# Kernel optimization log

Hardware: AMD Instinct MI355X
Metric: run time of the kernel (lower is better)

Reference implementation:

```python
import jax, jax.numpy as jnp
import numpy as np

NUM_BEAM, NUM_NULL, NUM_BIN, NUM_CH = 8, 4, 257, 8
NUM_BLOCK, NUM_FRAME = 8, 500
ALPHA, LOW_FREQ, HIGH_FREQ = 0.35, 5, 70


def setup_inputs() -> dict:
    key = jax.random.key(0)
    k1, k2, k3, k4 = jax.random.split(key, 4)
    return {
        "input": jax.random.normal(k1, (NUM_BLOCK, NUM_FRAME, 2, NUM_BIN, NUM_CH), jnp.float32),
        "beam_id": jax.random.randint(k2, (NUM_BLOCK,), 0, NUM_BEAM),
        "targ_w": jax.random.normal(k3, (NUM_BEAM, 2, NUM_BIN, NUM_CH), jnp.float32),
        "null_w": jax.random.normal(k4, (NUM_BEAM, NUM_NULL, 2, NUM_BIN, NUM_CH), jnp.float32),
    }


def _forward(input, beam_id, targ_w, null_w):
    a = ALPHA
    xr, xi = input[:, :, 0], input[:, :, 1]            # (B,T,F,C)
    # target beamformer: select per-block complex weights (B,2,F,C)
    tw = targ_w[beam_id]
    twr, twi = tw[:, 0], tw[:, 1]                      # (B,F,C)
    tr = jnp.einsum('btfc,bfc->btf', xr, twr) - jnp.einsum('btfc,bfc->btf', xi, twi)
    ti = jnp.einsum('btfc,bfc->btf', xr, twi) + jnp.einsum('btfc,bfc->btf', xi, twr)
    tr, ti = tr[..., None], ti[..., None]              # (B,T,F,1)
    # null beamformer: (B,N,2,F,C)
    nw = null_w[beam_id]
    nwr, nwi = nw[:, :, 0], nw[:, :, 1]                # (B,N,F,C)
    nr = jnp.einsum('btfc,bnfc->btfn', xr, nwr) - jnp.einsum('btfc,bnfc->btfn', xi, nwi)
    ni = jnp.einsum('btfc,bnfc->btfn', xr, nwi) + jnp.einsum('btfc,bnfc->btfn', xi, nwr)
    # elementwise cross-spectra products (B,T,F,N)
    pr = tr * nr + ti * ni
    pi = ti * nr - tr * ni
    pw = jnp.mean(xr ** 2 + xi ** 2, axis=-1, keepdims=True)  # (B,T,F,1)

    # t = 0 (note: (1-alpha) scales only the FIRST product, as in the source)
    phi_r0 = (1.0 - a) * tr[:, 0] * nr[:, 0] + ti[:, 0] * ni[:, 0]
    phi_i0 = (1.0 - a) * ti[:, 0] * nr[:, 0] - tr[:, 0] * ni[:, 0]
    psd0 = (1.0 - a) * pw[:, 0]
    phi0 = jnp.sqrt(phi_r0 ** 2 + phi_i0 ** 2)
    dcf0 = jnp.clip(phi0 / (psd0 + 1e-13), 0.01, 1.0)

    def step(carry, xs):
        phi_r, phi_i, psd = carry
        pr_t, pi_t, pw_t = xs
        phi_r = a * phi_r + (1.0 - a) * pr_t
        phi_i = a * phi_i + (1.0 - a) * pi_t
        psd = a * psd + (1.0 - a) * pw_t
        phi = jnp.sqrt(phi_r ** 2 + phi_i ** 2)
        dcf_t = jnp.clip(phi / (psd + 1e-13), 0.01, 1.0)
        pre = jnp.sum(psd[:, LOW_FREQ:HIGH_FREQ, :], axis=1, keepdims=True)
        aft = jnp.sum(phi[:, LOW_FREQ:HIGH_FREQ, :], axis=1, keepdims=True)
        ratio = jnp.clip(aft / (pre + 1e-10), 0.01, 1.0)
        dcf_t = jnp.sqrt(dcf_t * ratio)
        return (phi_r, phi_i, psd), dcf_t

    xs = (jnp.moveaxis(pr[:, 1:], 1, 0),
          jnp.moveaxis(pi[:, 1:], 1, 0),
          jnp.moveaxis(pw[:, 1:], 1, 0))
    _, dcf_rest = jax.lax.scan(step, (phi_r0, phi_i0, psd0), xs)  # (T-1,B,F,N)
    dcf = jnp.concatenate([dcf0[None], dcf_rest], axis=0)
    dcf = jnp.moveaxis(dcf, 0, 1)                                 # (B,T,F,N)
    targ_out = jnp.stack([tr[..., 0], ti[..., 0]], axis=2)        # (B,T,2,F)
    return dcf, targ_out


def reference(input, beam_id, targ_w, null_w):
    return _forward(input, beam_id, targ_w, null_w)
```

## Files before the change

kernel.cpp:

```cpp
#include <hip/hip_runtime.h>

#define NB 8
#define NT 500
#define NF 257
#define NC 8
#define NNUL 4
#define LOWF 5
#define HIGHF 70
#define S_CHUNK 8
#define WARM 4
#define N_CHUNK 63
#define AL 0.35f

__device__ __forceinline__ float dot4(const float4& a, const float4& b) {
    return a.x*b.x + a.y*b.y + a.z*b.z + a.w*b.w;
}
__device__ __forceinline__ float dot8(const float4& a0, const float4& a1,
                                      const float4& b0, const float4& b1) {
    return dot4(a0, b0) + dot4(a1, b1);
}
__device__ __forceinline__ float fast_rcp(float v) {
#if __has_builtin(__builtin_amdgcn_rcpf)
    return __builtin_amdgcn_rcpf(v);
#else
    return 1.0f / v;
#endif
}
__device__ __forceinline__ float fast_sqrt(float v) {
#if __has_builtin(__builtin_amdgcn_sqrtf)
    return __builtin_amdgcn_sqrtf(v);
#else
    return sqrtf(v);
#endif
}
__device__ __forceinline__ float clamp01(float v) {
#if __has_builtin(__builtin_amdgcn_fmed3f)
    return __builtin_amdgcn_fmed3f(v, 0.01f, 1.0f);
#else
    return fminf(fmaxf(v, 0.01f), 1.0f);
#endif
}

__global__ __launch_bounds__(1024, 4) void dcf_fused_kernel(
    const float* __restrict__ x,
    const int* __restrict__ beam_id,
    const float* __restrict__ targ_w,
    const float* __restrict__ null_w,
    float* __restrict__ out)
{
    const int tid = threadIdx.x;
    const int bid = blockIdx.x;
    const int b  = bid & 7;
    const int k  = bid >> 3;
    const int t0 = k * S_CHUNK;
    const int te = min(NT, t0 + S_CHUNK);
    int ts = t0 - WARM; if (ts < 0) ts = 0;

    const int f = tid >> 2;
    const int n = tid & 3;
    const int wid = tid >> 6;
    const int lane = tid & 63;
    const bool extra = (tid >= 1020);

    __shared__ float s_w256[16 + 4 * 16];
    __shared__ float s_xe[12 * 16];
    __shared__ float s_part[S_CHUNK][25];
    __shared__ float s_psd[S_CHUNK][260];
    __shared__ float s_dcf[S_CHUNK][1028];

    const int beam = beam_id[b];
    const int pA = n & 1;
    const int offA = pA * (NF * NC);
    const int offB = (1 - pA) * (NF * NC);
    const int psel = (n == 1 || n == 2) ? 1 : 0;
    const float nsign = pA ? -1.f : 1.f;
    const int rl = 2 * NF * NC;

    float4 tw0, tw1, w10, w11, w20, w21, w30, w31, w40, w41;
    {
        const float* tp = targ_w + ((size_t)(beam * 2 + psel) * NF + f) * NC;
        tw0 = *(const float4*)(tp);  tw1 = *(const float4*)(tp + 4);
        const float* qp  = null_w + ((size_t)((beam * NNUL + n) * 2) * NF + f) * NC;
        const float* qpx = null_w + ((size_t)((beam * NNUL + (n ^ 1)) * 2) * NF + f) * NC;
        w10 = *(const float4*)(qp  + offA);  w11 = *(const float4*)(qp  + offA + 4);
        w20 = *(const float4*)(qp  + offB);  w21 = *(const float4*)(qp  + offB + 4);
        w30 = *(const float4*)(qpx + offA);  w31 = *(const float4*)(qpx + offA + 4);
        w40 = *(const float4*)(qpx + offB);  w41 = *(const float4*)(qpx + offB + 4);
    }
    if (tid < 16) {
        int p = tid >> 3, c = tid & 7;
        s_w256[tid] = targ_w[((size_t)(beam * 2 + p) * NF + 256) * NC + c];
    } else if (tid < 80) {
        int i = tid - 16;
        int nn = i >> 4, p = (i >> 3) & 1, c = i & 7;
        s_w256[tid] = null_w[((size_t)((beam * NNUL + nn) * 2 + p) * NF + 256) * NC + c];
    } else if (tid >= 128 && tid < 176) {
        const int i = tid - 128;
        const int c = i >> 1, h = i & 1;
        const int fr = c >> 1, p = c & 1;
        if (fr < te - ts) {
            const float* src = x + (size_t)(b * NT + ts + fr) * rl
                             + p * (NF * NC) + 256 * NC + h * 4;
            *(float4*)&s_xe[fr * 16 + p * 8 + h * 4] = *(const float4*)src;
        }
    }
    __syncthreads();

    float phi_r = 0.f, phi_i = 0.f, psd = 0.f;
    float phi_r2 = 0.f, phi_i2 = 0.f, psd2 = 0.f;
    const float a = AL, oma = 1.0f - AL;

    const float* xpa = x + (size_t)(b * NT + ts) * rl + f * NC + offA;
    float4 pA0 = *(const float4*)(xpa);
    float4 pA1 = *(const float4*)(xpa + 4);

    float* outT = out + (size_t)NB * NT * NF * NNUL;
    float* poT = outT + ((size_t)(b * NT + t0) * 2 + n) * NF + f;
    float* sdp = &s_dcf[0][tid];
    float* spq = &s_psd[0][f];

    for (int t = ts; t < te; ++t) {
        const float4 A0 = pA0, A1 = pA1;
        xpa += rl;
        if (t + 1 < te) {
            pA0 = *(const float4*)(xpa);
            pA1 = *(const float4*)(xpa + 4);
        }

        const float d = dot8(A0, A1, tw0, tw1);
        const float e = __shfl_xor(d, 1);
        const float u = (n < 2) ? ((n == 0) ? (d - e) : (e - d)) : (d + e);
        const float v = __shfl_xor(u, 2);
        const float tr = (n < 2) ? u : v;
        const float ti = (n < 2) ? v : u;

        const float P  = dot8(A0, A1, w10, w11);
        const float X  = dot8(A0, A1, w20, w21);
        const float s3 = dot8(A0, A1, w30, w31);
        const float s4 = dot8(A0, A1, w40, w41);
        const float Q  = __shfl_xor(s3, 1);
        const float Y  = __shfl_xor(s4, 1);
        const float nr = nsign * (P - Q);
        const float ni = X + Y;

        float sq = dot4(A0, A0) + dot4(A1, A1);
        sq += __shfl_xor(sq, 1);
        const float pw = sq * 0.125f;

        if (t == 0) {
            phi_r = oma * tr * nr + ti * ni;
            phi_i = oma * ti * nr - tr * ni;
            psd   = oma * pw;
        } else {
            phi_r = a * phi_r + oma * (tr * nr + ti * ni);
            phi_i = a * phi_i + oma * (ti * nr - tr * ni);
            psd   = a * psd + oma * pw;
        }

        float tr2 = 0.f, ti2 = 0.f;
        if (extra) {
            const float* xe = &s_xe[(t - ts) * 16 + pA * 8];
            const float4 eA0 = *(const float4*)(xe);
            const float4 eA1 = *(const float4*)(xe + 4);
            const float4 etw0 = *(const float4*)&s_w256[psel * 8];
            const float4 etw1 = *(const float4*)&s_w256[psel * 8 + 4];
            const float* nq  = &s_w256[16 + n * 16];
            const float* nqx = &s_w256[16 + (n ^ 1) * 16];
            const float4 e10 = *(const float4*)(nq  + pA * 8);
            const float4 e11 = *(const float4*)(nq  + pA * 8 + 4);
            const float4 e20 = *(const float4*)(nq  + (1 - pA) * 8);
            const float4 e21 = *(const float4*)(nq  + (1 - pA) * 8 + 4);
            const float4 e30 = *(const float4*)(nqx + pA * 8);
            const float4 e31 = *(const float4*)(nqx + pA * 8 + 4);
            const float4 e40 = *(const float4*)(nqx + (1 - pA) * 8);
            const float4 e41 = *(const float4*)(nqx + (1 - pA) * 8 + 4);
            const float d2 = dot8(eA0, eA1, etw0, etw1);
            const float e2 = __shfl_xor(d2, 1);
            const float u2 = (n < 2) ? ((n == 0) ? (d2 - e2) : (e2 - d2)) : (d2 + e2);
            const float v2 = __shfl_xor(u2, 2);
            tr2 = (n < 2) ? u2 : v2;
            ti2 = (n < 2) ? v2 : u2;
            const float P2  = dot8(eA0, eA1, e10, e11);
            const float X2  = dot8(eA0, eA1, e20, e21);
            const float s32 = dot8(eA0, eA1, e30, e31);
            const float s42 = dot8(eA0, eA1, e40, e41);
            const float Q2  = __shfl_xor(s32, 1);
            const float Y2  = __shfl_xor(s42, 1);
            const float nr2 = nsign * (P2 - Q2);
            const float ni2 = X2 + Y2;
            float sq2 = dot4(eA0, eA0) + dot4(eA1, eA1);
            sq2 += __shfl_xor(sq2, 1);
            const float pw2 = sq2 * 0.125f;
            if (t == 0) {
                phi_r2 = oma * tr2 * nr2 + ti2 * ni2;
                phi_i2 = oma * ti2 * nr2 - tr2 * ni2;
                psd2   = oma * pw2;
            } else {
                phi_r2 = a * phi_r2 + oma * (tr2 * nr2 + ti2 * ni2);
                phi_i2 = a * phi_i2 + oma * (ti2 * nr2 - tr2 * ni2);
                psd2   = a * psd2 + oma * pw2;
            }
        }

        if (t >= t0) {
            const float phi = fast_sqrt(phi_r * phi_r + phi_i * phi_i);
            if (n < 2) *poT = (n == 0) ? tr : ti;
            *sdp = phi;
            if (n == 0) *spq = psd;
            if (extra) {
                const float phi2 = fast_sqrt(phi_r2 * phi_r2 + phi_i2 * phi_i2);
                sdp[4] = phi2;
                if (n == 0) spq[1] = psd2;
                if (n < 2) poT[1] = (n == 0) ? tr2 : ti2;
            }
            poT += 2 * NF; sdp += 1028; spq += 260;
        }
    }

    __syncthreads();

    const int nf = te - t0;
    if (wid < 8 && wid < nf && (t0 + wid) >= 1) {
        const int fr = wid;
        const float* sd = &s_dcf[fr][0];
        float vp = sd[20 + lane] + sd[84 + lane] + sd[148 + lane] + sd[212 + lane];
        if (lane < 4) vp += sd[276 + lane];
        const float* sp2 = &s_psd[fr][0];
        float vq = sp2[5 + lane];
        if (lane == 0) vq += sp2[69];
        vq += __shfl_xor(vq, 1);
        vq += __shfl_xor(vq, 2);
        #pragma unroll
        for (int off = 4; off < 64; off <<= 1) {
            vp += __shfl_xor(vp, off);
            vq += __shfl_xor(vq, off);
        }
        if (lane < 4)  s_part[fr][lane] = vp;
        if (lane == 0) s_part[fr][4]    = vq;
    }

    __syncthreads();

    float* po = out + ((size_t)(b * NT + t0) * NF + f) * NNUL + n;
    const float* sdr = &s_dcf[0][tid];
    const float* spr = &s_part[0][0];
    const float* sqr = &s_psd[0][f];
    for (int fr = 0; fr < nf; ++fr) {
        const int t = t0 + fr;
        float dcfv = clamp01(sdr[0] * fast_rcp(sqr[0] + 1e-13f));
        float dcf2v = 0.f;
        if (extra) dcf2v = clamp01(sdr[4] * fast_rcp(sqr[1] + 1e-13f));
        if (t >= 1) {
            const float pre = spr[4];
            const float aft = spr[n];
            const float ratio = clamp01(aft * fast_rcp(pre + 1e-10f));
            dcfv = fast_sqrt(dcfv * ratio);
            if (extra) dcf2v = fast_sqrt(dcf2v * ratio);
        }
        *po = dcfv;
        if (extra) po[NNUL] = dcf2v;
        po += NF * NNUL; sdr += 1028; spr += 25; sqr += 260;
    }
}

extern "C" void kernel_launch(void* const* d_in, const int* in_sizes, int n_in,
                              void* d_out, int out_size, void* d_ws, size_t ws_size,
                              hipStream_t stream) {
    const float* x       = (const float*)d_in[0];
    const int*   beam_id = (const int*)d_in[1];
    const float* targ_w  = (const float*)d_in[2];
    const float* null_w  = (const float*)d_in[3];
    float* out           = (float*)d_out;
    (void)d_ws; (void)ws_size;

    dcf_fused_kernel<<<dim3(NB * N_CHUNK), dim3(1024), 0, stream>>>(
        x, beam_id, targ_w, null_w, out);
}
```

Baseline: 127.0 us.

## Stage input frames via global_load_lds double buffer and store phi/psd in fp16 LDS

Replaces the per-thread register prefetch of each input frame with asynchronous global-to-LDS loads (global_load_lds) into a double buffer, waiting with vmcnt(1), so the next frame streams in while the current one is processed. Each thread then reads its channel slice from LDS. The shared buffers holding phi and psd between the recurrence and the reduction phase are also narrowed to _Float16, cutting LDS footprint and traffic. The fp16 storage loses precision (psd values may exceed fp16 range or lose accuracy), the extra 32KB of LDS may reduce occupancy, and the staging layout mapping is intricate.

```diff
diff --git a/kernel.cpp b/kernel.cpp
--- a/kernel.cpp
+++ b/kernel.cpp
@@ -11,6 +11,8 @@
 #define WARM 4
 #define N_CHUNK 63
 #define AL 0.35f
+
+#define HAVE_GLL __has_builtin(__builtin_amdgcn_global_load_lds)
 
 __device__ __forceinline__ float dot4(const float4& a, const float4& b) {
     return a.x*b.x + a.y*b.y + a.z*b.z + a.w*b.w;
@@ -62,11 +64,14 @@
     const int lane = tid & 63;
     const bool extra = (tid >= 1020);
 
-    __shared__ float s_w256[16 + 4 * 16];
-    __shared__ float s_xe[12 * 16];
-    __shared__ float s_part[S_CHUNK][25];
-    __shared__ float s_psd[S_CHUNK][260];
-    __shared__ float s_dcf[S_CHUNK][1028];
+    __shared__ float    s_w256[16 + 4 * 16];
+    __shared__ float    s_xe[12 * 16];
+    __shared__ float    s_part[S_CHUNK][25];
+    __shared__ _Float16 s_psd_h[S_CHUNK][260];
+    __shared__ _Float16 s_phi_h[S_CHUNK][1028];
+#if HAVE_GLL
+    __shared__ float    s_x[2][4096];
+#endif
 
     const int beam = beam_id[b];
     const int pA = n & 1;
@@ -110,22 +115,47 @@
     float phi_r2 = 0.f, phi_i2 = 0.f, psd2 = 0.f;
     const float a = AL, oma = 1.0f - AL;
 
+#if HAVE_GLL
+    typedef __attribute__((address_space(3))) void* as3_ptr;
+    typedef const __attribute__((address_space(1))) void* as1_ptr;
+    const int stage_off = wid * 128 + (lane & 31) * 4 + (lane >> 5) * (NF * NC);
+    const float* xs = x + (size_t)(b * NT + ts) * rl + stage_off;
+    char* ld0 = (char*)&s_x[0][0] + wid * 1024;
+    char* ld1 = ld0 + 16384;
+    __builtin_amdgcn_global_load_lds((as1_ptr)xs, (as3_ptr)ld0, 16, 0, 0);
+    xs += rl;
+    __builtin_amdgcn_global_load_lds((as1_ptr)xs, (as3_ptr)ld1, 16, 0, 0);
+    xs += rl;
+    const float* xr0 = &s_x[0][wid * 256 + pA * 128 + (f & 15) * 8];
+    const float* xr1 = xr0 + 4096;
+#else
     const float* xpa = x + (size_t)(b * NT + ts) * rl + f * NC + offA;
-    float4 pA0 = *(const float4*)(xpa);
-    float4 pA1 = *(const float4*)(xpa + 4);
+    float4 gA0 = *(const float4*)(xpa);
+    float4 gA1 = *(const float4*)(xpa + 4);
+#endif
 
     float* outT = out + (size_t)NB * NT * NF * NNUL;
     float* poT = outT + ((size_t)(b * NT + t0) * 2 + n) * NF + f;
-    float* sdp = &s_dcf[0][tid];
-    float* spq = &s_psd[0][f];
+    _Float16* sdp = &s_phi_h[0][tid];
+    _Float16* spq = &s_psd_h[0][f];
 
     for (int t = ts; t < te; ++t) {
-        const float4 A0 = pA0, A1 = pA1;
+#if HAVE_GLL
+        asm volatile("s_waitcnt vmcnt(1)" ::: "memory");
+#if __has_builtin(__builtin_amdgcn_sched_barrier)
+        __builtin_amdgcn_sched_barrier(0);
+#endif
+        const float* xr = ((t - ts) & 1) ? xr1 : xr0;
+        const float4 A0 = *(const float4*)(xr);
+        const float4 A1 = *(const float4*)(xr + 4);
+#else
+        const float4 A0 = gA0, A1 = gA1;
         xpa += rl;
         if (t + 1 < te) {
-            pA0 = *(const float4*)(xpa);
-            pA1 = *(const float4*)(xpa + 4);
-        }
+            gA0 = *(const float4*)(xpa);
+            gA1 = *(const float4*)(xpa + 4);
+        }
+#endif
 
         const float d = dot8(A0, A1, tw0, tw1);
         const float e = __shfl_xor(d, 1);
@@ -205,16 +235,24 @@
         if (t >= t0) {
             const float phi = fast_sqrt(phi_r * phi_r + phi_i * phi_i);
             if (n < 2) *poT = (n == 0) ? tr : ti;
-            *sdp = phi;
-            if (n == 0) *spq = psd;
+            *sdp = (_Float16)phi;
+            if (n == 0) *spq = (_Float16)psd;
             if (extra) {
                 const float phi2 = fast_sqrt(phi_r2 * phi_r2 + phi_i2 * phi_i2);
-                sdp[4] = phi2;
-                if (n == 0) spq[1] = psd2;
+                sdp[4] = (_Float16)phi2;
+                if (n == 0) spq[1] = (_Float16)psd2;
                 if (n < 2) poT[1] = (n == 0) ? tr2 : ti2;
             }
             poT += 2 * NF; sdp += 1028; spq += 260;
         }
+
+#if HAVE_GLL
+        if (t + 2 < te) {
+            char* ldn = ((t - ts) & 1) ? ld1 : ld0;
+            __builtin_amdgcn_global_load_lds((as1_ptr)xs, (as3_ptr)ldn, 16, 0, 0);
+            xs += rl;
+        }
+#endif
     }
 
     __syncthreads();
@@ -222,12 +260,13 @@
     const int nf = te - t0;
     if (wid < 8 && wid < nf && (t0 + wid) >= 1) {
         const int fr = wid;
-        const float* sd = &s_dcf[fr][0];
-        float vp = sd[20 + lane] + sd[84 + lane] + sd[148 + lane] + sd[212 + lane];
-        if (lane < 4) vp += sd[276 + lane];
-        const float* sp2 = &s_psd[fr][0];
-        float vq = sp2[5 + lane];
-        if (lane == 0) vq += sp2[69];
+        const _Float16* sd = &s_phi_h[fr][0];
+        float vp = (float)sd[20 + lane] + (float)sd[84 + lane]
+                 + (float)sd[148 + lane] + (float)sd[212 + lane];
+        if (lane < 4) vp += (float)sd[276 + lane];
+        const _Float16* sp2 = &s_psd_h[fr][0];
+        float vq = (float)sp2[5 + lane];
+        if (lane == 0) vq += (float)sp2[69];
         vq += __shfl_xor(vq, 1);
         vq += __shfl_xor(vq, 2);
         #pragma unroll
@@ -242,14 +281,14 @@
     __syncthreads();
 
     float* po = out + ((size_t)(b * NT + t0) * NF + f) * NNUL + n;
-    const float* sdr = &s_dcf[0][tid];
+    const _Float16* sdr = &s_phi_h[0][tid];
     const float* spr = &s_part[0][0];
-    const float* sqr = &s_psd[0][f];
+    const _Float16* sqr = &s_psd_h[0][f];
     for (int fr = 0; fr < nf; ++fr) {
         const int t = t0 + fr;
-        float dcfv = clamp01(sdr[0] * fast_rcp(sqr[0] + 1e-13f));
+        float dcfv = clamp01((float)sdr[0] * fast_rcp((float)sqr[0] + 1e-13f));
         float dcf2v = 0.f;
-        if (extra) dcf2v = clamp01(sdr[4] * fast_rcp(sqr[1] + 1e-13f));
+        if (extra) dcf2v = clamp01((float)sdr[4] * fast_rcp((float)sqr[1] + 1e-13f));
         if (t >= 1) {
             const float pre = spr[4];
             const float aft = spr[n];
```

Result: slower. 132.9 us (+4.7%).
